# Optimization experiments

Measured on AMD Instinct MI355X. Metric: run time of the kernel, lower is better.

Reference implementation:

```python
import jax, jax.numpy as jnp
import numpy as np

DIM = 768
HEADS = 12
HEAD_DIM = DIM // HEADS
SCALE = HEAD_DIM ** -0.5


def setup_inputs() -> dict:
    key = jax.random.key(0)
    ks = jax.random.split(key, 6)
    B, N, C = 2, 2048, DIM
    x = jax.random.normal(ks[0], (B, N, C), dtype=jnp.float32)
    s = C ** -0.5
    Wq = jax.random.normal(ks[1], (C, C), dtype=jnp.float32) * s
    Wk = jax.random.normal(ks[2], (C, C), dtype=jnp.float32) * s
    Wv = jax.random.normal(ks[3], (C, C), dtype=jnp.float32) * s
    Wp = jax.random.normal(ks[4], (C, C), dtype=jnp.float32) * s
    bp = jax.random.normal(ks[5], (C,), dtype=jnp.float32) * 0.01
    return {"x": x, "Wq": Wq, "Wk": Wk, "Wv": Wv, "Wp": Wp, "bp": bp}


def reference(x, Wq, Wk, Wv, Wp, bp):
    B, N, C = x.shape
    h, d = HEADS, HEAD_DIM
    # projections (no bias), split heads: (B, h, N, d)
    Q = (x @ Wq.T).reshape(B, N, h, d).transpose(0, 2, 1, 3)
    K = (x @ Wk.T).reshape(B, N, h, d).transpose(0, 2, 1, 3)
    V = (x @ Wv.T).reshape(B, N, h, d).transpose(0, 2, 1, 3)
    # averaged key: (B, h, 1, d) -> scores (B, h, N)
    K_avg = K.mean(axis=2)  # (B, h, d)
    z = jnp.einsum('bhnd,bhd->bhn', Q, K_avg) * SCALE
    attn = jax.nn.softmax(z, axis=-1)  # (B, h, N)
    # circulant gather: roll[b,h,i,j] = attn[b,h,(j-i)%N] / N
    idx = (jnp.arange(N)[None, :] - jnp.arange(N)[:, None]) % N  # (N, N)
    roll = attn[:, :, idx] / N  # (B, h, N, N)
    out = jnp.einsum('bhij,bhjd->bhid', roll, V)  # (B, h, N, d)
    out = out.transpose(0, 2, 1, 3).reshape(B, N, C)
    return out @ Wp.T + bp
```

## Files before the change

### kernel.cpp

```cpp
#include <hip/hip_runtime.h>


typedef __bf16 bf16x8 __attribute__((ext_vector_type(8)));
typedef float  f32x4  __attribute__((ext_vector_type(4)));

#define AS_GLOBAL(p) ((const __attribute__((address_space(1))) unsigned int*)(p))
#define AS_LDS(p)    ((__attribute__((address_space(3))) unsigned int*)(p))

__device__ __forceinline__ void async16(const void* g, void* l) {
    __builtin_amdgcn_global_load_lds(AS_GLOBAL(g), AS_LDS(l), 16, 0, 0);
}

#define WAITVM(N) asm volatile("s_waitcnt vmcnt(" #N ")" ::: "memory")
#define RAW_BARRIER() asm volatile("s_barrier" ::: "memory")

struct bf4 { __bf16 a, b, c, d; };

template <int MODE>
__device__ void gemm_phase(char* smem, const __bf16* __restrict__ A,
                           const __bf16* __restrict__ Bt, void* __restrict__ Cout,
                           const float* __restrict__ bias,
                           int K, int ldA, int ldBt, int ldC, int mBase, int nBase)
{
    constexpr int BM = 128, BN = 128, BK = 64;
    constexpr int BUF = (BM + BN) * BK * 2;
    const int tid = threadIdx.x;
    const int lane = tid & 63, wid = tid >> 6;
    const int lane15 = lane & 15, quad = lane >> 4;
    const int wm = (wid & 1) * 64, wn = (wid >> 1) * 64;

    auto stage = [&](int kb, char* buf) {
        __bf16* As = (__bf16*)buf;
        __bf16* Bs = As + BM * BK;
#pragma unroll
        for (int c0 = 0; c0 < BM * 8; c0 += 256) {
            int c = c0 + tid, row = c >> 3, slot = c & 7;
            int k8 = slot ^ (row & 7);
            async16(A + (size_t)(mBase + row) * ldA + kb + k8 * 8, As + c * 8);
        }
#pragma unroll
        for (int c0 = 0; c0 < BN * 8; c0 += 256) {
            int c = c0 + tid, row = c >> 3, slot = c & 7;
            int k8 = slot ^ (row & 7);
            async16(Bt + (size_t)(nBase + row) * ldBt + kb + k8 * 8, Bs + c * 8);
        }
    };

    f32x4 acc[4][4] = {};
    const int nk = K >> 6;
    char* p0 = smem;
    char* p1 = smem + BUF;
    char* p2 = smem + 2 * BUF;

    stage(0, p0);
    stage(64, p1);
    for (int ki = 0; ki < nk; ++ki) {
        if (ki + 1 < nk) { WAITVM(8); } else { WAITVM(0); }
        RAW_BARRIER();
        if (ki + 2 < nk) stage((ki + 2) << 6, p2);

        __bf16* As = (__bf16*)p0;
        __bf16* Bs = As + BM * BK;
#pragma unroll
        for (int ks = 0; ks < 2; ++ks) {
            bf16x8 af[4], bv[4];
#pragma unroll
            for (int mi = 0; mi < 4; ++mi) {
                int row = wm + mi * 16 + lane15;
                af[mi] = *(const bf16x8*)&As[row * 64 + ((ks * 4 + quad) ^ (row & 7)) * 8];
            }
#pragma unroll
            for (int ni = 0; ni < 4; ++ni) {
                int row = wn + ni * 16 + lane15;
                bv[ni] = *(const bf16x8*)&Bs[row * 64 + ((ks * 4 + quad) ^ (row & 7)) * 8];
            }
#pragma unroll
            for (int mi = 0; mi < 4; ++mi)
#pragma unroll
                for (int ni = 0; ni < 4; ++ni)
                    acc[mi][ni] = __builtin_amdgcn_mfma_f32_16x16x32_bf16(
                        af[mi], bv[ni], acc[mi][ni], 0, 0, 0);
        }
        char* t = p0; p0 = p1; p1 = p2; p2 = t;
    }

#pragma unroll
    for (int mi = 0; mi < 4; ++mi)
#pragma unroll
        for (int ni = 0; ni < 4; ++ni)
#pragma unroll
            for (int r = 0; r < 4; ++r) {
                int row = mBase + wm + mi * 16 + quad * 4 + r;
                int col = nBase + wn + ni * 16 + lane15;
                float v = acc[mi][ni][r];
                if (MODE == 0) {
                    ((__bf16*)Cout)[(size_t)row * ldC + col] = (__bf16)v;
                } else {
                    ((float*)Cout)[(size_t)row * ldC + col] = v + bias[col];
                }
            }
}

__global__ __launch_bounds__(256)
void k_prep(const float* __restrict__ x, const float* __restrict__ Wv,
            const float* __restrict__ Wp,
            __bf16* __restrict__ xb, __bf16* __restrict__ Wvb,
            __bf16* __restrict__ Wpb, float* __restrict__ x_part)
{
    const int bid = blockIdx.x, tid = threadIdx.x;

    const float4* xs = (const float4*)x + (size_t)bid * 1536;
    bf4* xd = (bf4*)xb + (size_t)bid * 1536;
#pragma unroll
    for (int r = 0; r < 6; ++r) {
        int j = tid + r * 256;
        float4 v = xs[j];
        xd[j] = bf4{(__bf16)v.x, (__bf16)v.y, (__bf16)v.z, (__bf16)v.w};
    }
    const float4* wv4 = (const float4*)Wv;  bf4* wvb4 = (bf4*)Wvb;
    const float4* wp4 = (const float4*)Wp;  bf4* wpb4 = (bf4*)Wpb;
    for (int t = tid; t < 288; t += 256) {
        int g = bid * 288 + t;
        float4 v = wv4[g];
        wvb4[g] = bf4{(__bf16)v.x, (__bf16)v.y, (__bf16)v.z, (__bf16)v.w};
        float4 w2 = wp4[g];
        wpb4[g] = bf4{(__bf16)w2.x, (__bf16)w2.y, (__bf16)w2.z, (__bf16)w2.w};
    }

    if (bid < 64) {
        const float* base = x + (size_t)bid * 64 * 768;
        float s0 = 0.f, s1 = 0.f, s2 = 0.f;
        for (int r = 0; r < 64; ++r) {
            const float* row = base + r * 768;
            s0 += row[tid];
            s1 += row[tid + 256];
            s2 += row[tid + 512];
        }
        x_part[bid * 768 + tid]       = s0;
        x_part[bid * 768 + tid + 256] = s1;
        x_part[bid * 768 + tid + 512] = s2;
    }
}

__global__ __launch_bounds__(256, 2)
void k_mid(const __bf16* __restrict__ xb, const __bf16* __restrict__ Wvb,
           const float* __restrict__ x_part, const float* __restrict__ Wk,
           const float* __restrict__ Wq,
           __bf16* __restrict__ VT, float* __restrict__ z_t)
{
    __shared__ __attribute__((aligned(16))) char smem[98304];
    const int bid = blockIdx.x;
    if (bid < 192) {
        gemm_phase<0>(smem, Wvb, xb, VT, nullptr, 768, 768, 768, 4096,
                      (bid / 32) * 128, (bid % 32) * 128);
        return;
    }
    const int tid = threadIdx.x;
    const int lane = tid & 63, wid = tid >> 6;
    const int idx = bid - 192;
    const int bh = idx >> 2, q = idx & 3;
    const int b = bh / 12, h = bh % 12;
    float* xa  = (float*)smem;
    float* uld = xa + 768;
    float* ka  = uld + 768;

    for (int c = tid; c < 768; c += 256) {
        float s = 0.f;
#pragma unroll
        for (int g = 0; g < 32; ++g) s += x_part[(b * 32 + g) * 768 + c];
        xa[c] = s;
    }
    __syncthreads();
    for (int round = 0; round < 16; ++round) {
        int o = round * 4 + wid;
        const float* wk = Wk + (size_t)(h * 64 + o) * 768;
        float s = 0.f;
#pragma unroll
        for (int c0 = 0; c0 < 768; c0 += 64) s += xa[c0 + lane] * wk[c0 + lane];
#pragma unroll
        for (int off = 32; off; off >>= 1) s += __shfl_down(s, off);
        if (lane == 0) ka[o] = s * (0.125f / 2048.f);
    }
    __syncthreads();
    for (int c = tid; c < 768; c += 256) {
        float s = 0.f;
#pragma unroll 16
        for (int d = 0; d < 64; ++d)
            s += ka[d] * Wq[(size_t)(h * 64 + d) * 768 + c];
        uld[c] = s;
    }
    __syncthreads();
    const int t0 = q * 512 + tid, t1 = t0 + 256;
    const bf16x8* r0 = (const bf16x8*)(xb + (size_t)(b * 2048 + t0) * 768);
    const bf16x8* r1 = (const bf16x8*)(xb + (size_t)(b * 2048 + t1) * 768);
    const float4* u4 = (const float4*)uld;
    float s0 = 0.f, s1 = 0.f;
#pragma unroll 8
    for (int j = 0; j < 96; ++j) {
        bf16x8 v0 = r0[j], v1 = r1[j];
        float4 ua = u4[j * 2], ub = u4[j * 2 + 1];
        s0 += (float)v0[0] * ua.x + (float)v0[1] * ua.y + (float)v0[2] * ua.z
            + (float)v0[3] * ua.w + (float)v0[4] * ub.x + (float)v0[5] * ub.y
            + (float)v0[6] * ub.z + (float)v0[7] * ub.w;
        s1 += (float)v1[0] * ua.x + (float)v1[1] * ua.y + (float)v1[2] * ua.z
            + (float)v1[3] * ua.w + (float)v1[4] * ub.x + (float)v1[5] * ub.y
            + (float)v1[6] * ub.z + (float)v1[7] * ub.w;
    }
    z_t[(size_t)bh * 2048 + t0] = s0;
    z_t[(size_t)bh * 2048 + t1] = s1;
}

__global__ __launch_bounds__(256, 2)
void k_conv(const float* __restrict__ z_t, const __bf16* __restrict__ VT,
            __bf16* __restrict__ outp)
{
    __shared__ __attribute__((aligned(16))) char smem[61568];
    __bf16 (*rep)[2056] = (__bf16(*)[2056])smem;
    __bf16* attn_s = (__bf16*)(smem + 32896);
    float* red = (float*)(smem + 36992);

    const int bid = blockIdx.x, tid = threadIdx.x;
    const int lane = tid & 63, wid = tid >> 6;
    const int lane15 = lane & 15, quad = lane >> 4;
    const int bh = bid >> 4, b = bh / 12, h = bh % 12;
    const int m0 = (bid & 15) * 128 + (wid & 1) * 64;
    const int wn = (wid >> 1) * 32;

    {
        const float* z = z_t + (size_t)bh * 2048;
        float v[8];
        float m = -1e30f;
#pragma unroll
        for (int j = 0; j < 8; ++j) { v[j] = z[tid + j * 256]; m = fmaxf(m, v[j]); }
#pragma unroll
        for (int off = 32; off; off >>= 1) m = fmaxf(m, __shfl_xor(m, off));
        if (lane == 0) red[wid] = m;
        __syncthreads();
        m = fmaxf(fmaxf(red[0], red[1]), fmaxf(red[2], red[3]));
        __syncthreads();
        float s = 0.f;
#pragma unroll
        for (int j = 0; j < 8; ++j) { v[j] = __expf(v[j] - m); s += v[j]; }
#pragma unroll
        for (int off = 32; off; off >>= 1) s += __shfl_xor(s, off);
        if (lane == 0) red[wid] = s;
        __syncthreads();
        s = red[0] + red[1] + red[2] + red[3];
        float inv = 1.f / (s * 2048.f);
#pragma unroll
        for (int j = 0; j < 8; ++j)
            attn_s[tid + j * 256] = (__bf16)(v[j] * inv);
    }
    __syncthreads();
    for (int idx = tid; idx < 8 * 2048; idx += 256) {
        int a = idx >> 11, u = idx & 2047;
        rep[a][u] = attn_s[(u + a) & 2047];
    }
    __syncthreads();

    const __bf16* vsrc = VT + (size_t)h * 64 * 4096 + b * 2048;

    auto stage = [&](int kb, char* buf) {
        __bf16* vt = (__bf16*)buf;
#pragma unroll
        for (int c0 = 0; c0 < 512; c0 += 256) {
            int c = c0 + tid, dd = c >> 3, slot = c & 7;
            int k8 = slot ^ (dd & 7);
            async16(vsrc + (size_t)dd * 4096 + kb * 64 + k8 * 8, vt + c * 8);
        }
    };

    f32x4 acc[4][2] = {};
    char* p0 = smem + 36992;
    char* p1 = p0 + 8192;
    char* p2 = p1 + 8192;
    stage(0, p0);
    stage(1, p1);
    for (int kb = 0; kb < 32; ++kb) {
        if (kb + 1 < 32) { WAITVM(2); } else { WAITVM(0); }
        RAW_BARRIER();
        if (kb + 2 < 32) stage(kb + 2, p2);
        __bf16* vt = (__bf16*)p0;

#pragma unroll
        for (int ks = 0; ks < 2; ++ks) {
            int kloc = ks * 32 + quad * 8;
            int kglob = kb * 64 + kloc;
            bf16x8 af[4], bv[2];
#pragma unroll
            for (int mi = 0; mi < 4; ++mi) {
                int m = m0 + mi * 16 + lane15;
                int p = (kglob - m) & 2047;
                int al = p & 7;
                af[mi] = *(const bf16x8*)&rep[al][p - al];
            }
#pragma unroll
            for (int ni = 0; ni < 2; ++ni) {
                int dd = wn + ni * 16 + lane15;
                int slot = (ks * 4 + quad) ^ (dd & 7);
                bv[ni] = *(const bf16x8*)&vt[dd * 64 + slot * 8];
            }
#pragma unroll
            for (int mi = 0; mi < 4; ++mi)
#pragma unroll
                for (int ni = 0; ni < 2; ++ni)
                    acc[mi][ni] = __builtin_amdgcn_mfma_f32_16x16x32_bf16(
                        af[mi], bv[ni], acc[mi][ni], 0, 0, 0);
        }
        char* t = p0; p0 = p1; p1 = p2; p2 = t;
    }

#pragma unroll
    for (int mi = 0; mi < 4; ++mi)
#pragma unroll
        for (int ni = 0; ni < 2; ++ni)
#pragma unroll
            for (int r = 0; r < 4; ++r) {
                int i = m0 + mi * 16 + quad * 4 + r;
                int dd = wn + ni * 16 + lane15;
                outp[(size_t)(b * 2048 + i) * 768 + h * 64 + dd] =
                    (__bf16)acc[mi][ni][r];
            }
}

__global__ __launch_bounds__(256, 2)
void k_out(const __bf16* __restrict__ out_pre, const __bf16* __restrict__ Wpb,
           const float* __restrict__ bp, float* __restrict__ out)
{
    __shared__ __attribute__((aligned(16))) char smem[98304];
    const int bid = blockIdx.x;
    gemm_phase<1>(smem, out_pre, Wpb, out, bp, 768, 768, 768, 768,
                  (bid / 6) * 128, (bid % 6) * 128);
}

extern "C" void kernel_launch(void* const* d_in, const int* in_sizes, int n_in,
                              void* d_out, int out_size, void* d_ws, size_t ws_size,
                              hipStream_t stream)
{
    (void)in_sizes; (void)n_in; (void)out_size; (void)ws_size;
    const float* x  = (const float*)d_in[0];
    const float* Wq = (const float*)d_in[1];
    const float* Wk = (const float*)d_in[2];
    const float* Wv = (const float*)d_in[3];
    const float* Wp = (const float*)d_in[4];
    const float* bp = (const float*)d_in[5];

    char* w = (char*)d_ws;
    auto alloc = [&](size_t bytes) {
        char* p = w; w += (bytes + 255) & ~(size_t)255; return p;
    };
    float*  x_part  = (float*) alloc((size_t)64 * 768 * 4);
    __bf16* xb      = (__bf16*)alloc((size_t)4096 * 768 * 2);
    __bf16* Wvb     = (__bf16*)alloc((size_t)768 * 768 * 2);
    __bf16* Wpb     = (__bf16*)alloc((size_t)768 * 768 * 2);
    float*  z_t     = (float*) alloc((size_t)24 * 2048 * 4);
    __bf16* VT      = (__bf16*)alloc((size_t)768 * 4096 * 2);
    __bf16* out_pre = (__bf16*)alloc((size_t)4096 * 768 * 2);

    k_prep<<<512, 256, 0, stream>>>(x, Wv, Wp, xb, Wvb, Wpb, x_part);
    k_mid <<<288, 256, 0, stream>>>(xb, Wvb, x_part, Wk, Wq, VT, z_t);
    k_conv<<<384, 256, 0, stream>>>(z_t, VT, out_pre);
    k_out <<<192, 256, 0, stream>>>(out_pre, Wpb, bp, (float*)d_out);
}
```

Baseline: 159.6 us.

## Compute attention scores with MFMA GEMM and split query-vector projection into its own kernel

The per-head query vector u (the averaged key pushed back through Wq) moves into a new small kernel, k_ub. It splits the Wq product across four blocks per head and writes the result as bf16. The score computation z = x·u, previously a scalar bf16 dot-product loop in 96 tail blocks of k_mid, becomes a skinny MFMA GEMM. That GEMM is a templated gemm_phase with BN=32 that writes only the valid per-batch columns, transposed into z_t. This removes the redundant u computation each tail block used to repeat and the slow scalar dot loop. The cost is an extra kernel launch, u rounded to bf16, and wasted MFMA work on unused columns, including the padding rows of Ub that are never initialised.

```diff
diff --git a/kernel.cpp b/kernel.cpp
--- a/kernel.cpp
+++ b/kernel.cpp
@@ -16,18 +16,19 @@
 
 struct bf4 { __bf16 a, b, c, d; };
 
-template <int MODE>
+template <int BN, int MODE>
 __device__ void gemm_phase(char* smem, const __bf16* __restrict__ A,
                            const __bf16* __restrict__ Bt, void* __restrict__ Cout,
                            const float* __restrict__ bias,
                            int K, int ldA, int ldBt, int ldC, int mBase, int nBase)
 {
-    constexpr int BM = 128, BN = 128, BK = 64;
+    constexpr int BM = 128, BK = 64;
     constexpr int BUF = (BM + BN) * BK * 2;
+    constexpr int WN = BN / 2, NI = WN / 16;
     const int tid = threadIdx.x;
     const int lane = tid & 63, wid = tid >> 6;
     const int lane15 = lane & 15, quad = lane >> 4;
-    const int wm = (wid & 1) * 64, wn = (wid >> 1) * 64;
+    const int wm = (wid & 1) * 64, wn = (wid >> 1) * WN;
 
     auto stage = [&](int kb, char* buf) {
         __bf16* As = (__bf16*)buf;
@@ -46,7 +47,7 @@
         }
     };
 
-    f32x4 acc[4][4] = {};
+    f32x4 acc[4][NI] = {};
     const int nk = K >> 6;
     char* p0 = smem;
     char* p1 = smem + BUF;
@@ -55,7 +56,9 @@
     stage(0, p0);
     stage(64, p1);
     for (int ki = 0; ki < nk; ++ki) {
-        if (ki + 1 < nk) { WAITVM(8); } else { WAITVM(0); }
+        if (ki + 1 < nk) {
+            if constexpr (BN == 128) { WAITVM(8); } else { WAITVM(5); }
+        } else { WAITVM(0); }
         RAW_BARRIER();
         if (ki + 2 < nk) stage((ki + 2) << 6, p2);
 
@@ -63,21 +66,21 @@
         __bf16* Bs = As + BM * BK;
 #pragma unroll
         for (int ks = 0; ks < 2; ++ks) {
-            bf16x8 af[4], bv[4];
+            bf16x8 af[4], bv[NI];
 #pragma unroll
             for (int mi = 0; mi < 4; ++mi) {
                 int row = wm + mi * 16 + lane15;
                 af[mi] = *(const bf16x8*)&As[row * 64 + ((ks * 4 + quad) ^ (row & 7)) * 8];
             }
 #pragma unroll
-            for (int ni = 0; ni < 4; ++ni) {
+            for (int ni = 0; ni < NI; ++ni) {
                 int row = wn + ni * 16 + lane15;
                 bv[ni] = *(const bf16x8*)&Bs[row * 64 + ((ks * 4 + quad) ^ (row & 7)) * 8];
             }
 #pragma unroll
             for (int mi = 0; mi < 4; ++mi)
 #pragma unroll
-                for (int ni = 0; ni < 4; ++ni)
+                for (int ni = 0; ni < NI; ++ni)
                     acc[mi][ni] = __builtin_amdgcn_mfma_f32_16x16x32_bf16(
                         af[mi], bv[ni], acc[mi][ni], 0, 0, 0);
         }
@@ -87,7 +90,7 @@
 #pragma unroll
     for (int mi = 0; mi < 4; ++mi)
 #pragma unroll
-        for (int ni = 0; ni < 4; ++ni)
+        for (int ni = 0; ni < NI; ++ni)
 #pragma unroll
             for (int r = 0; r < 4; ++r) {
                 int row = mBase + wm + mi * 16 + quad * 4 + r;
@@ -95,8 +98,12 @@
                 float v = acc[mi][ni][r];
                 if (MODE == 0) {
                     ((__bf16*)Cout)[(size_t)row * ldC + col] = (__bf16)v;
+                } else if (MODE == 1) {
+                    ((float*)Cout)[(size_t)row * ldC + col] = v + bias[col];
                 } else {
-                    ((float*)Cout)[(size_t)row * ldC + col] = v + bias[col];
+                    int b = row >> 11;
+                    if ((unsigned)(col - b * 12) < 12u)
+                        ((float*)Cout)[(size_t)col * 2048 + (row & 2047)] = v;
                 }
             }
 }
@@ -142,27 +149,16 @@
     }
 }
 
-__global__ __launch_bounds__(256, 2)
-void k_mid(const __bf16* __restrict__ xb, const __bf16* __restrict__ Wvb,
-           const float* __restrict__ x_part, const float* __restrict__ Wk,
-           const float* __restrict__ Wq,
-           __bf16* __restrict__ VT, float* __restrict__ z_t)
-{
-    __shared__ __attribute__((aligned(16))) char smem[98304];
-    const int bid = blockIdx.x;
-    if (bid < 192) {
-        gemm_phase<0>(smem, Wvb, xb, VT, nullptr, 768, 768, 768, 4096,
-                      (bid / 32) * 128, (bid % 32) * 128);
-        return;
-    }
-    const int tid = threadIdx.x;
+__global__ __launch_bounds__(256)
+void k_ub(const float* __restrict__ x_part, const float* __restrict__ Wk,
+          const float* __restrict__ Wq, __bf16* __restrict__ Ub)
+{
+    const int bid = blockIdx.x, tid = threadIdx.x;
     const int lane = tid & 63, wid = tid >> 6;
-    const int idx = bid - 192;
-    const int bh = idx >> 2, q = idx & 3;
+    const int bh = bid >> 2, q = bid & 3;
     const int b = bh / 12, h = bh % 12;
-    float* xa  = (float*)smem;
-    float* uld = xa + 768;
-    float* ka  = uld + 768;
+    __shared__ float xa[768];
+    __shared__ float ka[64];
 
     for (int c = tid; c < 768; c += 256) {
         float s = 0.f;
@@ -182,32 +178,30 @@
         if (lane == 0) ka[o] = s * (0.125f / 2048.f);
     }
     __syncthreads();
-    for (int c = tid; c < 768; c += 256) {
+    if (tid < 192) {
+        int c = q * 192 + tid;
         float s = 0.f;
 #pragma unroll 16
         for (int d = 0; d < 64; ++d)
             s += ka[d] * Wq[(size_t)(h * 64 + d) * 768 + c];
-        uld[c] = s;
-    }
-    __syncthreads();
-    const int t0 = q * 512 + tid, t1 = t0 + 256;
-    const bf16x8* r0 = (const bf16x8*)(xb + (size_t)(b * 2048 + t0) * 768);
-    const bf16x8* r1 = (const bf16x8*)(xb + (size_t)(b * 2048 + t1) * 768);
-    const float4* u4 = (const float4*)uld;
-    float s0 = 0.f, s1 = 0.f;
-#pragma unroll 8
-    for (int j = 0; j < 96; ++j) {
-        bf16x8 v0 = r0[j], v1 = r1[j];
-        float4 ua = u4[j * 2], ub = u4[j * 2 + 1];
-        s0 += (float)v0[0] * ua.x + (float)v0[1] * ua.y + (float)v0[2] * ua.z
-            + (float)v0[3] * ua.w + (float)v0[4] * ub.x + (float)v0[5] * ub.y
-            + (float)v0[6] * ub.z + (float)v0[7] * ub.w;
-        s1 += (float)v1[0] * ua.x + (float)v1[1] * ua.y + (float)v1[2] * ua.z
-            + (float)v1[3] * ua.w + (float)v1[4] * ub.x + (float)v1[5] * ub.y
-            + (float)v1[6] * ub.z + (float)v1[7] * ub.w;
-    }
-    z_t[(size_t)bh * 2048 + t0] = s0;
-    z_t[(size_t)bh * 2048 + t1] = s1;
+        Ub[(size_t)bh * 768 + c] = (__bf16)s;
+    }
+}
+
+__global__ __launch_bounds__(256, 2)
+void k_mid(const __bf16* __restrict__ xb, const __bf16* __restrict__ Wvb,
+           const __bf16* __restrict__ Ub,
+           __bf16* __restrict__ VT, float* __restrict__ z_t)
+{
+    __shared__ __attribute__((aligned(16))) char smem[98304];
+    const int bid = blockIdx.x;
+    if (bid < 192) {
+        gemm_phase<128, 0>(smem, Wvb, xb, VT, nullptr, 768, 768, 768, 4096,
+                           (bid / 32) * 128, (bid % 32) * 128);
+    } else {
+        gemm_phase<32, 2>(smem, xb, Ub, z_t, nullptr, 768, 768, 768, 0,
+                          (bid - 192) * 128, 0);
+    }
 }
 
 __global__ __launch_bounds__(256, 2)
@@ -329,8 +323,8 @@
 {
     __shared__ __attribute__((aligned(16))) char smem[98304];
     const int bid = blockIdx.x;
-    gemm_phase<1>(smem, out_pre, Wpb, out, bp, 768, 768, 768, 768,
-                  (bid / 6) * 128, (bid % 6) * 128);
+    gemm_phase<128, 1>(smem, out_pre, Wpb, out, bp, 768, 768, 768, 768,
+                       (bid / 6) * 128, (bid % 6) * 128);
 }
 
 extern "C" void kernel_launch(void* const* d_in, const int* in_sizes, int n_in,
@@ -353,12 +347,14 @@
     __bf16* xb      = (__bf16*)alloc((size_t)4096 * 768 * 2);
     __bf16* Wvb     = (__bf16*)alloc((size_t)768 * 768 * 2);
     __bf16* Wpb     = (__bf16*)alloc((size_t)768 * 768 * 2);
+    __bf16* Ub      = (__bf16*)alloc((size_t)32 * 768 * 2);
     float*  z_t     = (float*) alloc((size_t)24 * 2048 * 4);
     __bf16* VT      = (__bf16*)alloc((size_t)768 * 4096 * 2);
     __bf16* out_pre = (__bf16*)alloc((size_t)4096 * 768 * 2);
 
     k_prep<<<512, 256, 0, stream>>>(x, Wv, Wp, xb, Wvb, Wpb, x_part);
-    k_mid <<<288, 256, 0, stream>>>(xb, Wvb, x_part, Wk, Wq, VT, z_t);
+    k_ub  <<<96,  256, 0, stream>>>(x_part, Wk, Wq, Ub);
+    k_mid <<<224, 256, 0, stream>>>(xb, Wvb, Ub, VT, z_t);
     k_conv<<<384, 256, 0, stream>>>(z_t, VT, out_pre);
     k_out <<<192, 256, 0, stream>>>(out_pre, Wpb, bp, (float*)d_out);
 }
```

New measurement: 139.9 us. -12.3%, faster.
